# Performance work log

Measured on AMD Instinct MI355X. Metric: run time of the kernel, lower is better.

## Reference

```python
import jax, jax.numpy as jnp
import numpy as np

N = 25000      # nodes
E = 400000     # directed edges (avg degree 16)
F_IN = 133     # atom feature dim (QM_137k)
H = 8          # heads
C = 64         # hidden per head
HC = H * C     # 512
OUT = 1
NEG_SLOPE = 0.2
BN_EPS = 1e-5


def setup_inputs() -> dict:
    key = jax.random.key(0)
    ks = jax.random.split(key, 8)
    s = 0.05
    return {
        "x": jax.random.normal(ks[0], (N, F_IN), jnp.float32),
        "edge_index": jax.random.randint(ks[1], (2, E), 0, N, dtype=jnp.int32),
        # GATv2Conv params (share_weights=False): W_l for src, W_r for dst, att vector per head
        "Wl": jax.random.normal(ks[2], (F_IN, HC), jnp.float32) * s,
        "Wr": jax.random.normal(ks[3], (F_IN, HC), jnp.float32) * s,
        "att": jax.random.normal(ks[4], (H, C), jnp.float32) * s,
        "b1": jnp.zeros((HC,), jnp.float32),
        # BatchNorm1d (eval mode: running stats)
        "bn_gamma": jnp.ones((HC,), jnp.float32),
        "bn_beta": jnp.zeros((HC,), jnp.float32),
        "bn_mean": jnp.zeros((HC,), jnp.float32),
        "bn_var": jnp.ones((HC,), jnp.float32),
        # PReLU (default: single shared weight, init 0.25)
        "prelu_w": jnp.full((1,), 0.25, jnp.float32),
        # GCNConv params
        "Wg": jax.random.normal(ks[5], (HC, OUT), jnp.float32) * s,
        "bg": jnp.zeros((OUT,), jnp.float32),
    }


def _with_self_loops(edge_index):
    loops = jnp.arange(N, dtype=edge_index.dtype)
    src = jnp.concatenate([edge_index[0], loops])
    dst = jnp.concatenate([edge_index[1], loops])
    return src, dst


def _gatv2(x, edge_index, Wl, Wr, att, b1):
    # PyG GATv2Conv, concat=True, add_self_loops=True, eval (attention dropout off)
    src, dst = _with_self_loops(edge_index)
    xl = (x @ Wl).reshape(N, H, C)   # source-side transform
    xr = (x @ Wr).reshape(N, H, C)   # target-side transform
    msg = xl[src]                    # [E', H, C] gathered source messages
    e = jnp.einsum('ehc,hc->eh', jax.nn.leaky_relu(msg + xr[dst], NEG_SLOPE), att)  # [E', H]
    # segment softmax over incoming edges of each dst node (self loops => no empty segments)
    emax = jax.ops.segment_max(e, dst, num_segments=N)
    ee = jnp.exp(e - emax[dst])
    den = jax.ops.segment_sum(ee, dst, num_segments=N)
    agg = jax.ops.segment_sum(ee[:, :, None] * msg, dst, num_segments=N)  # [N, H, C]
    out = agg / den[:, :, None]
    return out.reshape(N, HC) + b1


def _gcn(x, edge_index, Wg, bg):
    # PyG GCNConv: add self loops, sym-normalized aggregation of x @ W, plus bias
    src, dst = _with_self_loops(edge_index)
    deg = jax.ops.segment_sum(jnp.ones_like(dst, dtype=x.dtype), dst, num_segments=N)
    dinv = jax.lax.rsqrt(jnp.maximum(deg, 1.0))
    h = x @ Wg                                   # [N, OUT]
    norm = dinv[src] * dinv[dst]                 # [E']
    return jax.ops.segment_sum(norm[:, None] * h[src], dst, num_segments=N) + bg


def reference(x, edge_index, Wl, Wr, att, b1, bn_gamma, bn_beta, bn_mean, bn_var,
              prelu_w, Wg, bg):
    h = _gatv2(x, edge_index, Wl, Wr, att, b1)
    # BatchNorm1d (eval) + PReLU
    h = (h - bn_mean) * jax.lax.rsqrt(bn_var + BN_EPS) * bn_gamma + bn_beta
    h = jnp.where(h >= 0, h, prelu_w * h)
    # dropout is identity in eval mode
    out = _gcn(h, edge_index, Wg, bg)
    return out.squeeze()  # [N]
```

## Files before the change

### kernel.cpp

```cpp
#include <hip/hip_runtime.h>

#define NN 25000
#define EE 400000
#define FIN 133
#define HCC 512
#define RPAD 25088
#define KPAD 160
#define NT 5
#define CAP 64
#define EPB 4082

typedef __attribute__((ext_vector_type(8))) __bf16 bf16x8;
typedef __attribute__((ext_vector_type(4))) float f32x4;
typedef __attribute__((ext_vector_type(8))) _Float16 f16x8;
typedef __attribute__((ext_vector_type(2))) _Float16 f16x2;

static __device__ __forceinline__ ushort f2bf(float f) {
    uint32_t u = __float_as_uint(f);
    uint32_t r = (u + 0x7fffu + ((u >> 16) & 1u)) >> 16;
    return (ushort)r;
}
static __device__ __forceinline__ float bf2f(ushort b) {
    return __uint_as_float(((uint32_t)b) << 16);
}

static __device__ __forceinline__ f16x2 lrelu2(f16x2 t) {
#if __has_builtin(__builtin_elementwise_max) && __has_builtin(__builtin_elementwise_min)
    const f16x2 z = {(_Float16)0.f, (_Float16)0.f};
    const f16x2 c = {(_Float16)0.2f, (_Float16)0.2f};
    return __builtin_elementwise_min(t, z) * c + __builtin_elementwise_max(t, z);
#else
    f16x2 r;
    r[0] = t[0] >= (_Float16)0.f ? t[0] : (_Float16)((float)t[0] * 0.2f);
    r[1] = t[1] >= (_Float16)0.f ? t[1] : (_Float16)((float)t[1] * 0.2f);
    return r;
#endif
}
static __device__ __forceinline__ float fdot2f(f16x2 a, f16x2 b, float c) {
#if __has_builtin(__builtin_amdgcn_fdot2)
    return __builtin_amdgcn_fdot2(a, b, c, false);
#else
    return c + (float)a[0] * (float)b[0] + (float)a[1] * (float)b[1];
#endif
}

__global__ __launch_bounds__(256) void k_prep(const float* __restrict__ x,
    const float* __restrict__ Wl, const float* __restrict__ Wr,
    ushort* __restrict__ ah, ushort* __restrict__ al,
    ushort* __restrict__ wh, ushort* __restrict__ wl,
    const int* __restrict__ srcp, const int* __restrict__ dstp,
    int* __restrict__ cnt, int* __restrict__ csr)
{
    const int tid = threadIdx.x;
    const int y = blockIdx.y;
    if (y == 21) {
        int e0 = blockIdx.x * EPB;
        int e1 = e0 + EPB; if (e1 > EE) e1 = EE;
        for (int e = e0 + tid; e < e1; e += 256) {
            int d = dstp[e];
            int pos = atomicAdd(&cnt[d], 1);
            csr[d * CAP + pos] = srcp[e];
        }
        return;
    }
    if (y < 20) {
        const int row = blockIdx.x * 256 + tid;
        const int oct = y;
        const int kb = oct * 8;
        ushort h[8], l[8];
        #pragma unroll
        for (int j = 0; j < 8; ++j) {
            int k = kb + j;
            float v = (row < NN && k < FIN) ? x[(size_t)row * FIN + k] : 0.f;
            ushort hh = f2bf(v);
            h[j] = hh;
            l[j] = f2bf(v - bf2f(hh));
        }
        uint4 H, L;
        H.x = h[0] | (h[1] << 16); H.y = h[2] | (h[3] << 16);
        H.z = h[4] | (h[5] << 16); H.w = h[6] | (h[7] << 16);
        L.x = l[0] | (l[1] << 16); L.y = l[2] | (l[3] << 16);
        L.z = l[4] | (l[5] << 16); L.w = l[6] | (l[7] << 16);
        size_t slot = (size_t)oct * RPAD + row;
        ((uint4*)ah)[slot] = H;
        ((uint4*)al)[slot] = L;
    } else {
        if (blockIdx.x >= 80) return;
        const int oct = blockIdx.x >> 2;
        const int col = (blockIdx.x & 3) * 256 + tid;
        const int kb = oct * 8;
        const float* W = (col < 512) ? Wl : Wr;
        const int c = (col < 512) ? col : col - 512;
        ushort h[8], l[8];
        #pragma unroll
        for (int j = 0; j < 8; ++j) {
            int k = kb + j;
            float v = (k < FIN) ? W[(size_t)k * 512 + c] : 0.f;
            ushort hh = f2bf(v);
            h[j] = hh;
            l[j] = f2bf(v - bf2f(hh));
        }
        uint4 H, L;
        H.x = h[0] | (h[1] << 16); H.y = h[2] | (h[3] << 16);
        H.z = h[4] | (h[5] << 16); H.w = h[6] | (h[7] << 16);
        L.x = l[0] | (l[1] << 16); L.y = l[2] | (l[3] << 16);
        L.z = l[4] | (l[5] << 16); L.w = l[6] | (l[7] << 16);
        size_t slot = (size_t)oct * 1024 + col;
        ((uint4*)wh)[slot] = H;
        ((uint4*)wl)[slot] = L;
    }
}

__global__ __launch_bounds__(256) void k_gemm3(
    const ushort* __restrict__ ah, const ushort* __restrict__ al,
    const ushort* __restrict__ wh, const ushort* __restrict__ wl,
    ushort* __restrict__ xl, ushort* __restrict__ xr)
{
    const int tid = threadIdx.x;
    const int wid = tid >> 6, lane = tid & 63;
    const int row0 = blockIdx.y * 128;
    const int cb = blockIdx.x * 128;
    const bool isR = cb >= 512;
    const int oc0 = isR ? cb - 512 : cb;
    const int wr = wid >> 1, wc = wid & 1;
    const int kg = lane >> 4, r = lane & 15;

    const int arow = row0 + wr * 64 + r;
    const int bcol = cb + wc * 64 + r;

    f32x4 acc[4][4];
    #pragma unroll
    for (int i = 0; i < 4; ++i)
        #pragma unroll
        for (int j = 0; j < 4; ++j) acc[i][j] = (f32x4)0.f;

    bf16x8 cah[2][4], cal[2][4], cbh[2][4], cbl[2][4];
    #pragma unroll
    for (int i = 0; i < 4; ++i) {
        const size_t abase = (size_t)kg * RPAD + arow;
        const size_t bbase = (size_t)kg * 1024 + bcol;
        cah[0][i] = ((const bf16x8*)ah)[abase + i * 16];
        cal[0][i] = ((const bf16x8*)al)[abase + i * 16];
        cbh[0][i] = ((const bf16x8*)wh)[bbase + i * 16];
        cbl[0][i] = ((const bf16x8*)wl)[bbase + i * 16];
    }
    #pragma unroll
    for (int t = 0; t < NT; ++t) {
        const int cur = t & 1, nxt = cur ^ 1;
        if (t + 1 < NT) {
            const size_t abase = (size_t)((t + 1) * 4 + kg) * RPAD + arow;
            const size_t bbase = (size_t)((t + 1) * 4 + kg) * 1024 + bcol;
            #pragma unroll
            for (int i = 0; i < 4; ++i) {
                cah[nxt][i] = ((const bf16x8*)ah)[abase + i * 16];
                cal[nxt][i] = ((const bf16x8*)al)[abase + i * 16];
                cbh[nxt][i] = ((const bf16x8*)wh)[bbase + i * 16];
                cbl[nxt][i] = ((const bf16x8*)wl)[bbase + i * 16];
            }
        }
        #pragma unroll
        for (int i = 0; i < 4; ++i)
            #pragma unroll
            for (int j = 0; j < 4; ++j)
                acc[i][j] = __builtin_amdgcn_mfma_f32_16x16x32_bf16(cah[cur][i], cbh[cur][j], acc[i][j], 0, 0, 0);
        #pragma unroll
        for (int i = 0; i < 4; ++i)
            #pragma unroll
            for (int j = 0; j < 4; ++j)
                acc[i][j] = __builtin_amdgcn_mfma_f32_16x16x32_bf16(cah[cur][i], cbl[cur][j], acc[i][j], 0, 0, 0);
        #pragma unroll
        for (int i = 0; i < 4; ++i)
            #pragma unroll
            for (int j = 0; j < 4; ++j)
                acc[i][j] = __builtin_amdgcn_mfma_f32_16x16x32_bf16(cal[cur][i], cbh[cur][j], acc[i][j], 0, 0, 0);
    }
    ushort* __restrict__ outp = isR ? xr : xl;
    const int cl = lane & 15, rq = lane >> 4;
    #pragma unroll
    for (int i = 0; i < 4; ++i) {
        #pragma unroll
        for (int rr = 0; rr < 4; ++rr) {
            int row = row0 + wr * 64 + i * 16 + rq * 4 + rr;
            if (row < NN) {
                #pragma unroll
                for (int j = 0; j < 4; ++j) {
                    _Float16 hv = (_Float16)acc[i][j][rr];
                    outp[(size_t)row * HCC + oc0 + wc * 64 + j * 16 + cl] =
                        *(const ushort*)&hv;
                }
            }
        }
    }
}

__global__ __launch_bounds__(256) void k_gat(
    const ushort* __restrict__ xl, const ushort* __restrict__ xr,
    const float* __restrict__ att, const float* __restrict__ b1,
    const float* __restrict__ gam, const float* __restrict__ bet,
    const float* __restrict__ mean, const float* __restrict__ var,
    const float* __restrict__ pw, const float* __restrict__ Wg,
    const int* __restrict__ cnt, const int* __restrict__ csr,
    float* __restrict__ g, float* __restrict__ dinvp)
{
    const int lane = threadIdx.x & 63;
    const int node = blockIdx.x * 4 + (threadIdx.x >> 6);
    const int sb = lane * 8;
    f16x8 xv = *(const f16x8*)&xr[(size_t)node * HCC + sb];
    float4 a0 = *(const float4*)&att[sb];
    float4 a1 = *(const float4*)&att[sb + 4];
    f16x2 xrh[4], avh[4];
    {
        const f16x2* xp = (const f16x2*)&xv;
        xrh[0] = xp[0]; xrh[1] = xp[1]; xrh[2] = xp[2]; xrh[3] = xp[3];
    }
    avh[0] = {(_Float16)a0.x, (_Float16)a0.y};
    avh[1] = {(_Float16)a0.z, (_Float16)a0.w};
    avh[2] = {(_Float16)a1.x, (_Float16)a1.y};
    avh[3] = {(_Float16)a1.z, (_Float16)a1.w};
    float s = 0.f;
    float acc[8] = {0.f, 0.f, 0.f, 0.f, 0.f, 0.f, 0.f, 0.f};
    const int deg = cnt[node];
    const int beg = node * CAP;
    auto process = [&](f16x8 hv) {
        const f16x2* hp = (const f16x2*)&hv;
        float ep = 0.f;
        #pragma unroll
        for (int p = 0; p < 4; ++p) {
            f16x2 t = hp[p] + xrh[p];
            ep = fdot2f(lrelu2(t), avh[p], ep);
        }
        ep += __shfl_xor(ep, 1);
        ep += __shfl_xor(ep, 2);
        ep += __shfl_xor(ep, 4);
        float w = __expf(ep);
        s += w;
        const _Float16* he = (const _Float16*)&hv;
        #pragma unroll
        for (int k = 0; k < 8; ++k) acc[k] += w * (float)he[k];
    };
    auto row = [&](int srcn) -> f16x8 {
        return *(const f16x8*)&xl[(size_t)srcn * HCC + sb];
    };
    process(row(node));
    int j = 0;
    for (; j + 4 <= deg; j += 4) {
        int sA = csr[beg + j], sB = csr[beg + j + 1];
        int sC = csr[beg + j + 2], sD = csr[beg + j + 3];
        f16x8 hA = row(sA);
        f16x8 hB = row(sB);
        f16x8 hC = row(sC);
        f16x8 hD = row(sD);
        process(hA); process(hB); process(hC); process(hD);
    }
    for (; j < deg; ++j) process(row(csr[beg + j]));
    float inv = 1.f / s;
    float p_w = pw[0];
    float dot = 0.f;
    #pragma unroll
    for (int k = 0; k < 8; ++k) {
        int idx = sb + k;
        float v = acc[k] * inv + b1[idx];
        v = (v - mean[idx]) * rsqrtf(var[idx] + 1e-5f) * gam[idx] + bet[idx];
        v = v >= 0.f ? v : p_w * v;
        dot += v * Wg[idx];
    }
    dot += __shfl_xor(dot, 1);
    dot += __shfl_xor(dot, 2);
    dot += __shfl_xor(dot, 4);
    dot += __shfl_xor(dot, 8);
    dot += __shfl_xor(dot, 16);
    dot += __shfl_xor(dot, 32);
    if (lane == 0) {
        float dn = rsqrtf((float)(deg + 1));
        g[node] = dn * dot;
        dinvp[node] = dn;
    }
}

__global__ __launch_bounds__(256) void k_gcn(
    const float* __restrict__ g, const float* __restrict__ dinv,
    const int* __restrict__ cnt, const int* __restrict__ csr,
    const float* __restrict__ bg, float* __restrict__ out)
{
    int t = blockIdx.x * 256 + threadIdx.x;
    int node = t >> 2;
    int sub = t & 3;
    if (node >= NN) return;
    int deg = cnt[node];
    int base = node * CAP;
    float s = 0.f;
    for (int j = sub; j < deg; j += 4) s += g[csr[base + j]];
    s += __shfl_xor(s, 1);
    s += __shfl_xor(s, 2);
    if (sub == 0) out[node] = dinv[node] * (g[node] + s) + bg[0];
}

extern "C" void kernel_launch(void* const* d_in, const int* in_sizes, int n_in,
                              void* d_out, int out_size, void* d_ws, size_t ws_size,
                              hipStream_t stream)
{
    const float* x    = (const float*)d_in[0];
    const int*   ei   = (const int*)d_in[1];
    const float* Wl   = (const float*)d_in[2];
    const float* Wr   = (const float*)d_in[3];
    const float* att  = (const float*)d_in[4];
    const float* b1   = (const float*)d_in[5];
    const float* gam  = (const float*)d_in[6];
    const float* bet  = (const float*)d_in[7];
    const float* mean = (const float*)d_in[8];
    const float* var  = (const float*)d_in[9];
    const float* pw   = (const float*)d_in[10];
    const float* Wg   = (const float*)d_in[11];
    const float* bg   = (const float*)d_in[12];
    float* out = (float*)d_out;

    char* base = (char*)d_ws;
    size_t o = 0;
    ushort* xl  = (ushort*)(base + o); o += (size_t)NN * HCC * 2;
    ushort* xr  = (ushort*)(base + o); o += (size_t)NN * HCC * 2;
    o = (o + 15) & ~(size_t)15;
    float* g    = (float*)(base + o); o += NN * 4;
    float* dinv = (float*)(base + o); o += NN * 4;
    int*   cnt  = (int*)(base + o);   o += NN * 4;
    int*   csr  = (int*)(base + o);   o += (size_t)NN * CAP * 4;
    o = (o + 15) & ~(size_t)15;
    ushort* ah = (ushort*)(base + o); o += (size_t)RPAD * KPAD * 2;
    ushort* al = (ushort*)(base + o); o += (size_t)RPAD * KPAD * 2;
    ushort* wh = (ushort*)(base + o); o += (size_t)KPAD * 1024 * 2;
    ushort* wl = (ushort*)(base + o); o += (size_t)KPAD * 1024 * 2;

    const int* srcp = ei;
    const int* dstp = ei + EE;

    hipMemsetAsync(cnt, 0, NN * sizeof(int), stream);
    k_prep<<<dim3(98, 22), 256, 0, stream>>>(x, Wl, Wr, ah, al, wh, wl,
                                             srcp, dstp, cnt, csr);
    k_gemm3<<<dim3(8, 196), 256, 0, stream>>>(ah, al, wh, wl, xl, xr);
    k_gat<<<NN / 4, 256, 0, stream>>>(xl, xr, att, b1, gam, bet, mean, var, pw, Wg,
                                      cnt, csr, g, dinv);
    k_gcn<<<(NN * 4 + 255) / 256, 256, 0, stream>>>(g, dinv, cnt, csr, bg, out);
}
```

Baseline: 229.0 us.

## Permute GEMM output columns for vector stores and fold BN constants

The GEMM epilogue now writes four adjacent fp16 values per row with one 8-byte store instead of four scattered 2-byte stores, which permutes the xl/xr column order within each 64-column head. To stay consistent, the prep kernel writes permuted copies of att and Wg and precomputes the fused bias+BatchNorm scale and shift per channel, so the GAT kernel loads fewer parameter arrays and does less per-channel arithmetic. This adds one extra small grid row to the prep kernel and relies on the permutation being correct everywhere xl and xr are consumed.

```diff
diff --git a/kernel.cpp b/kernel.cpp
--- a/kernel.cpp
+++ b/kernel.cpp
@@ -13,6 +13,7 @@
 typedef __attribute__((ext_vector_type(8))) __bf16 bf16x8;
 typedef __attribute__((ext_vector_type(4))) float f32x4;
 typedef __attribute__((ext_vector_type(8))) _Float16 f16x8;
+typedef __attribute__((ext_vector_type(4))) _Float16 f16x4;
 typedef __attribute__((ext_vector_type(2))) _Float16 f16x2;
 
 static __device__ __forceinline__ ushort f2bf(float f) {
@@ -49,10 +50,29 @@
     ushort* __restrict__ ah, ushort* __restrict__ al,
     ushort* __restrict__ wh, ushort* __restrict__ wl,
     const int* __restrict__ srcp, const int* __restrict__ dstp,
-    int* __restrict__ cnt, int* __restrict__ csr)
+    int* __restrict__ cnt, int* __restrict__ csr,
+    const float* __restrict__ att, const float* __restrict__ b1,
+    const float* __restrict__ gam, const float* __restrict__ bet,
+    const float* __restrict__ mean, const float* __restrict__ var,
+    const float* __restrict__ Wg,
+    float* __restrict__ attP, float* __restrict__ AP,
+    float* __restrict__ BP, float* __restrict__ WgP)
 {
     const int tid = threadIdx.x;
     const int y = blockIdx.y;
+    if (y == 22) {
+        if (blockIdx.x >= 2) return;
+        int p = blockIdx.x * 256 + tid;
+        int g = p >> 6, s = p & 63;
+        int cl = s >> 2, j = s & 3;
+        int c = (g << 6) | (j << 4) | cl;
+        float sc = gam[c] * rsqrtf(var[c] + 1e-5f);
+        attP[p] = att[c];
+        AP[p] = sc;
+        BP[p] = b1[c] * sc + (bet[c] - mean[c] * sc);
+        WgP[p] = Wg[c];
+        return;
+    }
     if (y == 21) {
         int e0 = blockIdx.x * EPB;
         int e1 = e0 + EPB; if (e1 > EE) e1 = EE;
@@ -176,18 +196,17 @@
     }
     ushort* __restrict__ outp = isR ? xr : xl;
     const int cl = lane & 15, rq = lane >> 4;
+    const int scol = oc0 + wc * 64 + cl * 4;
     #pragma unroll
     for (int i = 0; i < 4; ++i) {
         #pragma unroll
         for (int rr = 0; rr < 4; ++rr) {
             int row = row0 + wr * 64 + i * 16 + rq * 4 + rr;
             if (row < NN) {
+                f16x4 hv;
                 #pragma unroll
-                for (int j = 0; j < 4; ++j) {
-                    _Float16 hv = (_Float16)acc[i][j][rr];
-                    outp[(size_t)row * HCC + oc0 + wc * 64 + j * 16 + cl] =
-                        *(const ushort*)&hv;
-                }
+                for (int j = 0; j < 4; ++j) hv[j] = (_Float16)acc[i][j][rr];
+                *(f16x4*)&outp[(size_t)row * HCC + scol] = hv;
             }
         }
     }
@@ -195,10 +214,9 @@
 
 __global__ __launch_bounds__(256) void k_gat(
     const ushort* __restrict__ xl, const ushort* __restrict__ xr,
-    const float* __restrict__ att, const float* __restrict__ b1,
-    const float* __restrict__ gam, const float* __restrict__ bet,
-    const float* __restrict__ mean, const float* __restrict__ var,
-    const float* __restrict__ pw, const float* __restrict__ Wg,
+    const float* __restrict__ attP, const float* __restrict__ AP,
+    const float* __restrict__ BP, const float* __restrict__ WgP,
+    const float* __restrict__ pw,
     const int* __restrict__ cnt, const int* __restrict__ csr,
     float* __restrict__ g, float* __restrict__ dinvp)
 {
@@ -206,8 +224,8 @@
     const int node = blockIdx.x * 4 + (threadIdx.x >> 6);
     const int sb = lane * 8;
     f16x8 xv = *(const f16x8*)&xr[(size_t)node * HCC + sb];
-    float4 a0 = *(const float4*)&att[sb];
-    float4 a1 = *(const float4*)&att[sb + 4];
+    float4 a0 = *(const float4*)&attP[sb];
+    float4 a1 = *(const float4*)&attP[sb + 4];
     f16x2 xrh[4], avh[4];
     {
         const f16x2* xp = (const f16x2*)&xv;
@@ -259,10 +277,9 @@
     #pragma unroll
     for (int k = 0; k < 8; ++k) {
         int idx = sb + k;
-        float v = acc[k] * inv + b1[idx];
-        v = (v - mean[idx]) * rsqrtf(var[idx] + 1e-5f) * gam[idx] + bet[idx];
+        float v = (acc[k] * inv) * AP[idx] + BP[idx];
         v = v >= 0.f ? v : p_w * v;
-        dot += v * Wg[idx];
+        dot += v * WgP[idx];
     }
     dot += __shfl_xor(dot, 1);
     dot += __shfl_xor(dot, 2);
@@ -323,6 +340,10 @@
     float* dinv = (float*)(base + o); o += NN * 4;
     int*   cnt  = (int*)(base + o);   o += NN * 4;
     int*   csr  = (int*)(base + o);   o += (size_t)NN * CAP * 4;
+    float* attP = (float*)(base + o); o += HCC * 4;
+    float* AP   = (float*)(base + o); o += HCC * 4;
+    float* BP   = (float*)(base + o); o += HCC * 4;
+    float* WgP  = (float*)(base + o); o += HCC * 4;
     o = (o + 15) & ~(size_t)15;
     ushort* ah = (ushort*)(base + o); o += (size_t)RPAD * KPAD * 2;
     ushort* al = (ushort*)(base + o); o += (size_t)RPAD * KPAD * 2;
@@ -333,10 +354,12 @@
     const int* dstp = ei + EE;
 
     hipMemsetAsync(cnt, 0, NN * sizeof(int), stream);
-    k_prep<<<dim3(98, 22), 256, 0, stream>>>(x, Wl, Wr, ah, al, wh, wl,
-                                             srcp, dstp, cnt, csr);
+    k_prep<<<dim3(98, 23), 256, 0, stream>>>(x, Wl, Wr, ah, al, wh, wl,
+                                             srcp, dstp, cnt, csr,
+                                             att, b1, gam, bet, mean, var, Wg,
+                                             attP, AP, BP, WgP);
     k_gemm3<<<dim3(8, 196), 256, 0, stream>>>(ah, al, wh, wl, xl, xr);
-    k_gat<<<NN / 4, 256, 0, stream>>>(xl, xr, att, b1, gam, bet, mean, var, pw, Wg,
+    k_gat<<<NN / 4, 256, 0, stream>>>(xl, xr, attP, AP, BP, WgP, pw,
                                       cnt, csr, g, dinv);
     k_gcn<<<(NN * 4 + 255) / 256, 256, 0, stream>>>(g, dinv, cnt, csr, bg, out);
 }
```

After: 222.5 us. -2.9%, faster.
